# Kernel tuning notes

Measured on AMD Instinct MI355X. Metric: run time of the kernel, lower is better.

## Reference

```python
import jax, jax.numpy as jnp
import numpy as np

B, D, T, H = 256, 256, 512, 512  # batch, input_dim, seq_len, hidden_dim


def setup_inputs() -> dict:
    key = jax.random.key(0)
    ks = jax.random.split(key, 7)
    s = 1.0 / np.sqrt(H)
    u = lambda k, shape: jax.random.uniform(k, shape, jnp.float32, -s, s)
    return {
        "x": jax.random.normal(ks[0], (B, D, T), jnp.float32),
        "W_ih": u(ks[1], (4 * H, D)),   # gate order: i, f, g, o (PyTorch)
        "W_hh": u(ks[2], (4 * H, H)),
        "b_ih": u(ks[3], (4 * H,)),
        "b_hh": u(ks[4], (4 * H,)),
        "W_mlp": u(ks[5], (1, H)),      # Linear(hidden_dim, num_classes=1)
        "b_mlp": u(ks[6], (1,)),
    }


def reference(x, W_ih, W_hh, b_ih, b_hh, W_mlp, b_mlp):
    # x: (B, D, T) -> (T, B, D), matching the two transposes in LSTM_model
    xs = jnp.transpose(x, (2, 0, 1))
    # Precompute input contributions for all timesteps: (T, B, 4H)
    x_gates = jnp.einsum('tbd,gd->tbg', xs, W_ih) + b_ih + b_hh
    Hh = W_hh.shape[1]

    def step(carry, xg):
        h, c = carry
        g = xg + h @ W_hh.T                      # (B, 4H)
        i = jax.nn.sigmoid(g[:, 0 * Hh:1 * Hh])
        f = jax.nn.sigmoid(g[:, 1 * Hh:2 * Hh])
        gg = jnp.tanh(g[:, 2 * Hh:3 * Hh])
        o = jax.nn.sigmoid(g[:, 3 * Hh:4 * Hh])
        c_new = f * c + i * gg
        h_new = o * jnp.tanh(c_new)
        return (h_new, c_new), h_new

    h0 = jnp.zeros((x.shape[0], Hh), x.dtype)
    c0 = jnp.zeros((x.shape[0], Hh), x.dtype)
    _, h_t = jax.lax.scan(step, (h0, c0), x_gates)   # (T, B, H)

    # MLP with num_layers=1: single Linear(H, 1) then sigmoid, per timestep.
    logits = jnp.einsum('tbh,h->tb', h_t, W_mlp[0]) + b_mlp[0]  # (T, B)
    out = jax.nn.sigmoid(logits)
    return out.T  # (B, T), matching out[..., t] layout
```

## Files before the change

### kernel.cpp

```cpp
#include <hip/hip_runtime.h>
#include <stdint.h>

#define BSZ 256
#define DIN 256
#define TLEN 512
#define HDIM 512
#define POISON 0xAAAAAAAAu

typedef _Float16 h16;
typedef unsigned int u32;
typedef unsigned long long u64;
typedef __attribute__((ext_vector_type(8))) _Float16 half8;
typedef __attribute__((ext_vector_type(4))) float f32x4;

__device__ __forceinline__ float fast_sigmoid(float x) {
    return 1.0f / (1.0f + __expf(-x));
}
__device__ __forceinline__ float fast_tanh(float x) {
    return 2.0f / (1.0f + __expf(-2.0f * x)) - 1.0f;
}

__device__ __forceinline__ u64 load_agent_u64(const u64* p) {
    return __hip_atomic_load((u64*)p, __ATOMIC_RELAXED, __HIP_MEMORY_SCOPE_AGENT);
}
__device__ __forceinline__ void store_agent_u32(u32* p, u32 v) {
    __hip_atomic_store(p, v, __ATOMIC_RELAXED, __HIP_MEMORY_SCOPE_AGENT);
}

__global__ __launch_bounds__(256)
void transpose_x(const float* __restrict__ x, h16* __restrict__ xT) {
    __shared__ h16 tl[64][72];
    const int tid = threadIdx.x;
    const int tb  = blockIdx.x & 7;
    const int bd0 = (blockIdx.x >> 3) * 64;
    const int t0  = tb * 64;
#pragma unroll
    for (int p = 0; p < 4; ++p) {
        int idx  = p * 256 + tid;
        int bd_l = idx >> 4;
        int t4   = idx & 15;
        float4 v = *(const float4*)(x + (size_t)(bd0 + bd_l) * TLEN + t0 + t4 * 4);
        tl[t4 * 4 + 0][bd_l] = (h16)v.x;
        tl[t4 * 4 + 1][bd_l] = (h16)v.y;
        tl[t4 * 4 + 2][bd_l] = (h16)v.z;
        tl[t4 * 4 + 3][bd_l] = (h16)v.w;
    }
    __syncthreads();
#pragma unroll
    for (int p = 0; p < 2; ++p) {
        int idx = p * 256 + tid;
        int t_l = idx >> 3;
        int seg = idx & 7;
        uint4 v = *(const uint4*)&tl[t_l][seg * 8];
        *(uint4*)(xT + (size_t)(t0 + t_l) * (BSZ * DIN) + bd0 + seg * 8) = v;
    }
}

__global__ __launch_bounds__(256, 1)
void lstm_kernel(const float* __restrict__ x,
                 const float* __restrict__ W_ih,
                 const float* __restrict__ W_hh,
                 const float* __restrict__ b_ih,
                 const float* __restrict__ b_hh,
                 const float* __restrict__ W_mlp,
                 const h16* __restrict__ xT,
                 int use_xT,
                 h16* __restrict__ hslots,
                 float* __restrict__ logits,
                 float* __restrict__ part,
                 int use_part)
{
    __shared__ h16  h_sw[16][64][8];
    __shared__ h16  x_sw[8][8][64][8];
    __shared__ float g_lds[16][132];

    const int tid  = threadIdx.x;
    const int bid  = blockIdx.x;
    const int clique = bid & 15;
    const int mem    = bid >> 4;
    const int lane = tid & 63;
    const int w    = tid >> 6;
    const int l15  = lane & 15;
    const int lq   = lane >> 4;
    const int cb   = clique * 16;

    half8 whh[2][16], wih[2][8];
#pragma unroll
    for (int i = 0; i < 2; ++i) {
        const int nrow = w * HDIM + mem * 32 + i * 16 + l15;
        const float* wr = W_hh + (size_t)nrow * HDIM;
#pragma unroll
        for (int kk = 0; kk < 16; ++kk) {
            const float* p = wr + kk * 32 + lq * 8;
            half8 v;
#pragma unroll
            for (int j = 0; j < 8; ++j) v[j] = (h16)p[j];
            whh[i][kk] = v;
        }
        const float* wr2 = W_ih + (size_t)nrow * DIN;
#pragma unroll
        for (int kk = 0; kk < 8; ++kk) {
            const float* p = wr2 + kk * 32 + lq * 8;
            half8 v;
#pragma unroll
            for (int j = 0; j < 8; ++j) v[j] = (h16)p[j];
            wih[i][kk] = v;
        }
    }

    const int eb = tid >> 4;
    const int ej = tid & 15;
    const int jg = mem * 32 + ej * 2;
    float bias[8];
#pragma unroll
    for (int q = 0; q < 4; ++q) {
        bias[q * 2 + 0] = b_ih[q * HDIM + jg]     + b_hh[q * HDIM + jg];
        bias[q * 2 + 1] = b_ih[q * HDIM + jg + 1] + b_hh[q * HDIM + jg + 1];
    }
    const float wm0 = W_mlp[jg], wm1 = W_mlp[jg + 1];
    float c0 = 0.0f, c1 = 0.0f;
    float pbuf[8];

    u32  qoff[8];
    h16* hdst4[4];
#pragma unroll
    for (int it = 0; it < 4; ++it) {
        int c   = it * 256 + tid;
        int L   = c & 63;
        int kk  = c >> 6;
        int b   = L & 15;
        int k0  = kk * 32 + (L >> 4) * 8;
        qoff[it * 2 + 0] = (u32)((b * HDIM + k0) >> 2);
        qoff[it * 2 + 1] = qoff[it * 2 + 0] + 1;
        hdst4[it] = &h_sw[kk][L][0];
    }
    const size_t own_off = (size_t)(cb + eb) * HDIM + jg;

    for (int t = 0; t < TLEN; ++t) {
        if (use_xT) {
#pragma unroll
            for (int it = 0; it < 2; ++it) {
                int c  = it * 256 + tid;
                int L  = c & 63;
                int kk = c >> 6;
                int b  = L & 15;
                int d0 = kk * 32 + (L >> 4) * 8;
                uint4 v = *(const uint4*)(xT + (size_t)t * (BSZ * DIN)
                                             + (size_t)(cb + b) * DIN + d0);
                *(uint4*)&x_sw[0][kk][L][0] = v;
            }
        } else if ((t & 7) == 0) {
            const int d   = tid;
            const int kk  = d >> 5;
            const int dlq = (d >> 3) & 3;
            const int j   = d & 7;
#pragma unroll 4
            for (int b = 0; b < 16; ++b) {
                const float* p = x + ((size_t)(cb + b) * DIN + d) * TLEN + t;
                float4 v0 = *(const float4*)p;
                float4 v1 = *(const float4*)(p + 4);
                int L = b | (dlq << 4);
                x_sw[0][kk][L][j] = (h16)v0.x;
                x_sw[1][kk][L][j] = (h16)v0.y;
                x_sw[2][kk][L][j] = (h16)v0.z;
                x_sw[3][kk][L][j] = (h16)v0.w;
                x_sw[4][kk][L][j] = (h16)v1.x;
                x_sw[5][kk][L][j] = (h16)v1.y;
                x_sw[6][kk][L][j] = (h16)v1.z;
                x_sw[7][kk][L][j] = (h16)v1.w;
            }
        }
        const int sb = use_xT ? 0 : (t & 7);

        if (t > 0) {
            asm volatile("s_waitcnt vmcnt(0)" ::: "memory");
            store_agent_u32((u32*)(hslots + (size_t)((t + 3) & 7) * BSZ * HDIM
                                          + own_off), POISON);

            const u64* hb = (const u64*)(hslots + ((size_t)(t & 7) * BSZ + cb) * HDIM);
            u64 q[8];
            u32 pend = 0xFFu;
            while (pend) {
#pragma unroll
                for (int i = 0; i < 8; ++i)
                    if (pend & (1u << i)) q[i] = load_agent_u64(hb + qoff[i]);
                u32 np = 0;
#pragma unroll
                for (int i = 0; i < 8; ++i)
                    if (pend & (1u << i)) {
                        u32 lo = (u32)q[i], hi = (u32)(q[i] >> 32);
                        if (lo == POISON || hi == POISON) np |= 1u << i;
                    }
                pend = np;
                if (pend) __builtin_amdgcn_s_sleep(1);
            }
#pragma unroll
            for (int it = 0; it < 4; ++it) {
                union { u64 qq[2]; uint4 v; } pk;
                pk.qq[0] = q[it * 2 + 0];
                pk.qq[1] = q[it * 2 + 1];
                *(uint4*)hdst4[it] = pk.v;
            }
        }
        __syncthreads();

        f32x4 acc0 = {0.f, 0.f, 0.f, 0.f};
        f32x4 acc1 = {0.f, 0.f, 0.f, 0.f};
#pragma unroll
        for (int kk = 0; kk < 8; ++kk) {
            half8 a = *(const half8*)&x_sw[sb][kk][lane][0];
            acc0 = __builtin_amdgcn_mfma_f32_16x16x32_f16(a, wih[0][kk], acc0, 0, 0, 0);
            acc1 = __builtin_amdgcn_mfma_f32_16x16x32_f16(a, wih[1][kk], acc1, 0, 0, 0);
        }
        if (t > 0) {
#pragma unroll
            for (int kk = 0; kk < 16; ++kk) {
                half8 a = *(const half8*)&h_sw[kk][lane][0];
                acc0 = __builtin_amdgcn_mfma_f32_16x16x32_f16(a, whh[0][kk], acc0, 0, 0, 0);
                acc1 = __builtin_amdgcn_mfma_f32_16x16x32_f16(a, whh[1][kk], acc1, 0, 0, 0);
            }
        }
        {
            const int col0 = w * 32 + l15;
            const int col1 = w * 32 + 16 + l15;
#pragma unroll
            for (int r = 0; r < 4; ++r) {
                g_lds[lq * 4 + r][col0] = acc0[r];
                g_lds[lq * 4 + r][col1] = acc1[r];
            }
        }
        __syncthreads();

        float mlp_p;
        {
            float gi0 = g_lds[eb][ej * 2]          + bias[0];
            float gi1 = g_lds[eb][ej * 2 + 1]      + bias[1];
            float gf0 = g_lds[eb][32 + ej * 2]     + bias[2];
            float gf1 = g_lds[eb][32 + ej * 2 + 1] + bias[3];
            float gg0 = g_lds[eb][64 + ej * 2]     + bias[4];
            float gg1 = g_lds[eb][64 + ej * 2 + 1] + bias[5];
            float go0 = g_lds[eb][96 + ej * 2]     + bias[6];
            float go1 = g_lds[eb][96 + ej * 2 + 1] + bias[7];
            c0 = fast_sigmoid(gf0) * c0 + fast_sigmoid(gi0) * fast_tanh(gg0);
            c1 = fast_sigmoid(gf1) * c1 + fast_sigmoid(gi1) * fast_tanh(gg1);
            float h0 = fast_sigmoid(go0) * fast_tanh(c0);
            float h1 = fast_sigmoid(go1) * fast_tanh(c1);

            union { h16 h2[2]; u32 uu; } pk;
            pk.h2[0] = (h16)h0; pk.h2[1] = (h16)h1;
            if (pk.uu == POISON) pk.uu ^= 1u;
            store_agent_u32((u32*)(hslots + (size_t)((t + 1) & 7) * BSZ * HDIM
                                          + own_off), pk.uu);

            float p = h0 * wm0 + h1 * wm1;
            p += __shfl_xor(p, 1);
            p += __shfl_xor(p, 2);
            p += __shfl_xor(p, 4);
            p += __shfl_xor(p, 8);
            mlp_p = p;
            pbuf[t & 7] = p;
            if (use_part && (t & 7) == 7 && ej == 0) {
                float* pd = &part[((size_t)mem * BSZ + cb + eb) * TLEN + (t - 7)];
                float4 v0, v1;
                v0.x = pbuf[0]; v0.y = pbuf[1]; v0.z = pbuf[2]; v0.w = pbuf[3];
                v1.x = pbuf[4]; v1.y = pbuf[5]; v1.z = pbuf[6]; v1.w = pbuf[7];
                *(float4*)pd       = v0;
                *(float4*)(pd + 4) = v1;
            }
        }
        if (!use_part && ej == 0) {
            atomicAdd(&logits[(size_t)(cb + eb) * TLEN + t], mlp_p);
        }
    }
}

__global__ __launch_bounds__(256)
void final_sigmoid(const float* __restrict__ logits,
                   const float* __restrict__ part,
                   int use_part,
                   const float* __restrict__ b_mlp,
                   float* __restrict__ out) {
    int i = blockIdx.x * 256 + threadIdx.x;
    float v;
    if (use_part) {
        int t = i & (TLEN - 1);
        int b = i >> 9;
        v = 0.f;
#pragma unroll
        for (int mm = 0; mm < 16; ++mm)
            v += part[((size_t)mm * BSZ + b) * TLEN + t];
    } else {
        v = logits[i];
    }
    v += b_mlp[0];
    out[i] = 1.0f / (1.0f + __expf(-v));
}

extern "C" void kernel_launch(void* const* d_in, const int* in_sizes, int n_in,
                              void* d_out, int out_size, void* d_ws, size_t ws_size,
                              hipStream_t stream) {
    const float* x     = (const float*)d_in[0];
    const float* W_ih  = (const float*)d_in[1];
    const float* W_hh  = (const float*)d_in[2];
    const float* b_ih  = (const float*)d_in[3];
    const float* b_hh  = (const float*)d_in[4];
    const float* W_mlp = (const float*)d_in[5];
    const float* b_mlp = (const float*)d_in[6];
    float* out = (float*)d_out;

    char* ws = (char*)d_ws;
    float* logits = (float*)ws;
    h16*   hslots = (h16*)(ws + 1048576);
    float* part   = (float*)(ws + 4194304);
    h16*   xT     = (h16*)(ws + 20971520);
    const int use_part = (ws_size >= (size_t)20971520) ? 1 : 0;
    const int use_xT   = (ws_size >= (size_t)88080384) ? 1 : 0;

    hipMemsetAsync(d_ws, 0, 524288, stream);

    if (use_xT) {
        transpose_x<<<8192, 256, 0, stream>>>(x, xT);
    }
    lstm_kernel<<<256, 256, 0, stream>>>(x, W_ih, W_hh, b_ih, b_hh, W_mlp,
                                         xT, use_xT, hslots, logits,
                                         part, use_part);
    final_sigmoid<<<(BSZ * TLEN) / 256, 256, 0, stream>>>(logits, part, use_part,
                                                          b_mlp, out);
}
```

Measured before the change: 2.108 ms.

## Remap gate rows so MFMA output yields LSTM cell update in registers

Reorders the W_hh/W_ih rows each wave loads so that one wave's MFMA accumulators hold all four gates for a set of hidden units. The cell update is then done in registers with lane shuffles instead of spilling gates to LDS and re-reading them after a barrier. It also removes the pre-transposed x path and the per-clique partial-logit buffer, always using the strided x loads and atomic logit accumulation. Finally it moves the h-slot poll ahead of the x load and issues the poison stores after the h publish. The cost is more atomics, the reinstated strided x reads, and an extra barrier after the MFMAs.

```diff
diff --git a/kernel.cpp b/kernel.cpp
--- a/kernel.cpp
+++ b/kernel.cpp
@@ -13,11 +13,11 @@
 typedef __attribute__((ext_vector_type(8))) _Float16 half8;
 typedef __attribute__((ext_vector_type(4))) float f32x4;
 
-__device__ __forceinline__ float fast_sigmoid(float x) {
-    return 1.0f / (1.0f + __expf(-x));
-}
-__device__ __forceinline__ float fast_tanh(float x) {
-    return 2.0f / (1.0f + __expf(-2.0f * x)) - 1.0f;
+__device__ __forceinline__ float fsigm(float x) {
+    return __fdividef(1.0f, 1.0f + __expf(-x));
+}
+__device__ __forceinline__ float ftanh(float x) {
+    return __fdividef(2.0f, 1.0f + __expf(-2.0f * x)) - 1.0f;
 }
 
 __device__ __forceinline__ u64 load_agent_u64(const u64* p) {
@@ -25,35 +25,6 @@
 }
 __device__ __forceinline__ void store_agent_u32(u32* p, u32 v) {
     __hip_atomic_store(p, v, __ATOMIC_RELAXED, __HIP_MEMORY_SCOPE_AGENT);
-}
-
-__global__ __launch_bounds__(256)
-void transpose_x(const float* __restrict__ x, h16* __restrict__ xT) {
-    __shared__ h16 tl[64][72];
-    const int tid = threadIdx.x;
-    const int tb  = blockIdx.x & 7;
-    const int bd0 = (blockIdx.x >> 3) * 64;
-    const int t0  = tb * 64;
-#pragma unroll
-    for (int p = 0; p < 4; ++p) {
-        int idx  = p * 256 + tid;
-        int bd_l = idx >> 4;
-        int t4   = idx & 15;
-        float4 v = *(const float4*)(x + (size_t)(bd0 + bd_l) * TLEN + t0 + t4 * 4);
-        tl[t4 * 4 + 0][bd_l] = (h16)v.x;
-        tl[t4 * 4 + 1][bd_l] = (h16)v.y;
-        tl[t4 * 4 + 2][bd_l] = (h16)v.z;
-        tl[t4 * 4 + 3][bd_l] = (h16)v.w;
-    }
-    __syncthreads();
-#pragma unroll
-    for (int p = 0; p < 2; ++p) {
-        int idx = p * 256 + tid;
-        int t_l = idx >> 3;
-        int seg = idx & 7;
-        uint4 v = *(const uint4*)&tl[t_l][seg * 8];
-        *(uint4*)(xT + (size_t)(t0 + t_l) * (BSZ * DIN) + bd0 + seg * 8) = v;
-    }
 }
 
 __global__ __launch_bounds__(256, 1)
@@ -63,16 +34,13 @@
                  const float* __restrict__ b_ih,
                  const float* __restrict__ b_hh,
                  const float* __restrict__ W_mlp,
-                 const h16* __restrict__ xT,
-                 int use_xT,
                  h16* __restrict__ hslots,
-                 float* __restrict__ logits,
-                 float* __restrict__ part,
-                 int use_part)
+                 float* __restrict__ logits)
 {
-    __shared__ h16  h_sw[16][64][8];
-    __shared__ h16  x_sw[8][8][64][8];
-    __shared__ float g_lds[16][132];
+    __shared__ h16 h_sw[16][64][8];
+    __shared__ h16 x_sw[8][8][64][8];
+    __shared__ h16 pad[2048];
+    if (blockIdx.x == 0xFFFFFFFu) pad[threadIdx.x] = (h16)0.f;
 
     const int tid  = threadIdx.x;
     const int bid  = blockIdx.x;
@@ -83,11 +51,16 @@
     const int l15  = lane & 15;
     const int lq   = lane >> 4;
     const int cb   = clique * 16;
+    const int half = l15 >> 3;
+    const int uo   = l15 & 7;
+    const int u    = mem * 32 + w * 8 + uo;
+    const bool is_even = (uo & 1) == 0;
 
     half8 whh[2][16], wih[2][8];
 #pragma unroll
     for (int i = 0; i < 2; ++i) {
-        const int nrow = w * HDIM + mem * 32 + i * 16 + l15;
+        const int gate = i * 2 + half;
+        const int nrow = gate * HDIM + mem * 32 + w * 8 + uo;
         const float* wr = W_hh + (size_t)nrow * HDIM;
 #pragma unroll
         for (int kk = 0; kk < 16; ++kk) {
@@ -108,18 +81,15 @@
         }
     }
 
-    const int eb = tid >> 4;
-    const int ej = tid & 15;
-    const int jg = mem * 32 + ej * 2;
-    float bias[8];
-#pragma unroll
-    for (int q = 0; q < 4; ++q) {
-        bias[q * 2 + 0] = b_ih[q * HDIM + jg]     + b_hh[q * HDIM + jg];
-        bias[q * 2 + 1] = b_ih[q * HDIM + jg + 1] + b_hh[q * HDIM + jg + 1];
-    }
-    const float wm0 = W_mlp[jg], wm1 = W_mlp[jg + 1];
-    float c0 = 0.0f, c1 = 0.0f;
-    float pbuf[8];
+    const float bi = b_ih[u]            + b_hh[u];
+    const float bf = b_ih[HDIM + u]     + b_hh[HDIM + u];
+    const float bg = b_ih[2 * HDIM + u] + b_hh[2 * HDIM + u];
+    const float bo = b_ih[3 * HDIM + u] + b_hh[3 * HDIM + u];
+    const float wm = W_mlp[u];
+    const int   b0 = lq * 4 + half * 2;
+    const size_t own0 = (size_t)(cb + b0) * HDIM + u;
+    const size_t own1 = (size_t)(cb + b0 + 1) * HDIM + u;
+    float cst0 = 0.0f, cst1 = 0.0f;
 
     u32  qoff[8];
     h16* hdst4[4];
@@ -134,22 +104,36 @@
         qoff[it * 2 + 1] = qoff[it * 2 + 0] + 1;
         hdst4[it] = &h_sw[kk][L][0];
     }
-    const size_t own_off = (size_t)(cb + eb) * HDIM + jg;
 
     for (int t = 0; t < TLEN; ++t) {
-        if (use_xT) {
-#pragma unroll
-            for (int it = 0; it < 2; ++it) {
-                int c  = it * 256 + tid;
-                int L  = c & 63;
-                int kk = c >> 6;
-                int b  = L & 15;
-                int d0 = kk * 32 + (L >> 4) * 8;
-                uint4 v = *(const uint4*)(xT + (size_t)t * (BSZ * DIN)
-                                             + (size_t)(cb + b) * DIN + d0);
-                *(uint4*)&x_sw[0][kk][L][0] = v;
-            }
-        } else if ((t & 7) == 0) {
+        u64 q[8];
+        if (t > 0) {
+            const u64* hb = (const u64*)(hslots + ((size_t)(t & 7) * BSZ + cb) * HDIM);
+            u32 pend = 0xFFu;
+            while (pend) {
+#pragma unroll
+                for (int i = 0; i < 8; ++i)
+                    if (pend & (1u << i)) q[i] = load_agent_u64(hb + qoff[i]);
+                u32 np = 0;
+#pragma unroll
+                for (int i = 0; i < 8; ++i)
+                    if (pend & (1u << i)) {
+                        u32 lo = (u32)q[i], hi = (u32)(q[i] >> 32);
+                        if (lo == POISON || hi == POISON) np |= 1u << i;
+                    }
+                pend = np;
+                if (pend) __builtin_amdgcn_s_sleep(1);
+            }
+#pragma unroll
+            for (int it = 0; it < 4; ++it) {
+                union { u64 qq[2]; uint4 v; } pk;
+                pk.qq[0] = q[it * 2 + 0];
+                pk.qq[1] = q[it * 2 + 1];
+                *(uint4*)hdst4[it] = pk.v;
+            }
+        }
+
+        if ((t & 7) == 0) {
             const int d   = tid;
             const int kk  = d >> 5;
             const int dlq = (d >> 3) & 3;
@@ -170,38 +154,7 @@
                 x_sw[7][kk][L][j] = (h16)v1.w;
             }
         }
-        const int sb = use_xT ? 0 : (t & 7);
-
-        if (t > 0) {
-            asm volatile("s_waitcnt vmcnt(0)" ::: "memory");
-            store_agent_u32((u32*)(hslots + (size_t)((t + 3) & 7) * BSZ * HDIM
-                                          + own_off), POISON);
-
-            const u64* hb = (const u64*)(hslots + ((size_t)(t & 7) * BSZ + cb) * HDIM);
-            u64 q[8];
-            u32 pend = 0xFFu;
-            while (pend) {
-#pragma unroll
-                for (int i = 0; i < 8; ++i)
-                    if (pend & (1u << i)) q[i] = load_agent_u64(hb + qoff[i]);
-                u32 np = 0;
-#pragma unroll
-                for (int i = 0; i < 8; ++i)
-                    if (pend & (1u << i)) {
-                        u32 lo = (u32)q[i], hi = (u32)(q[i] >> 32);
-                        if (lo == POISON || hi == POISON) np |= 1u << i;
-                    }
-                pend = np;
-                if (pend) __builtin_amdgcn_s_sleep(1);
-            }
-#pragma unroll
-            for (int it = 0; it < 4; ++it) {
-                union { u64 qq[2]; uint4 v; } pk;
-                pk.qq[0] = q[it * 2 + 0];
-                pk.qq[1] = q[it * 2 + 1];
-                *(uint4*)hdst4[it] = pk.v;
-            }
-        }
+        const int sb = t & 7;
         __syncthreads();
 
         f32x4 acc0 = {0.f, 0.f, 0.f, 0.f};
@@ -220,79 +173,67 @@
                 acc1 = __builtin_amdgcn_mfma_f32_16x16x32_f16(a, whh[1][kk], acc1, 0, 0, 0);
             }
         }
+        __syncthreads();
+
+        float oa0 = half ? acc0[2] : acc0[0];
+        float oa1 = half ? acc0[3] : acc0[1];
+        float ob0 = half ? acc1[2] : acc1[0];
+        float ob1 = half ? acc1[3] : acc1[1];
+        float s0 = __shfl_xor(half ? acc0[0] : acc0[2], 8);
+        float s1 = __shfl_xor(half ? acc0[1] : acc0[3], 8);
+        float s2 = __shfl_xor(half ? acc1[0] : acc1[2], 8);
+        float s3 = __shfl_xor(half ? acc1[1] : acc1[3], 8);
+        float gi0 = half ? s0 : oa0,  gf0 = half ? oa0 : s0;
+        float gg0 = half ? s2 : ob0,  go0 = half ? ob0 : s2;
+        float gi1 = half ? s1 : oa1,  gf1 = half ? oa1 : s1;
+        float gg1 = half ? s3 : ob1,  go1 = half ? ob1 : s3;
+
+        float iv0 = fsigm(gi0 + bi), fv0 = fsigm(gf0 + bf);
+        float gv0 = ftanh(gg0 + bg), ov0 = fsigm(go0 + bo);
+        cst0 = fv0 * cst0 + iv0 * gv0;
+        float h0 = ov0 * ftanh(cst0);
+        float iv1 = fsigm(gi1 + bi), fv1 = fsigm(gf1 + bf);
+        float gv1 = ftanh(gg1 + bg), ov1 = fsigm(go1 + bo);
+        cst1 = fv1 * cst1 + iv1 * gv1;
+        float h1 = ov1 * ftanh(cst1);
+
+        float hp0 = __shfl_xor(h0, 1);
+        float hp1 = __shfl_xor(h1, 1);
+
+        asm volatile("s_waitcnt vmcnt(0)" ::: "memory");
         {
-            const int col0 = w * 32 + l15;
-            const int col1 = w * 32 + 16 + l15;
-#pragma unroll
-            for (int r = 0; r < 4; ++r) {
-                g_lds[lq * 4 + r][col0] = acc0[r];
-                g_lds[lq * 4 + r][col1] = acc1[r];
-            }
-        }
-        __syncthreads();
-
-        float mlp_p;
-        {
-            float gi0 = g_lds[eb][ej * 2]          + bias[0];
-            float gi1 = g_lds[eb][ej * 2 + 1]      + bias[1];
-            float gf0 = g_lds[eb][32 + ej * 2]     + bias[2];
-            float gf1 = g_lds[eb][32 + ej * 2 + 1] + bias[3];
-            float gg0 = g_lds[eb][64 + ej * 2]     + bias[4];
-            float gg1 = g_lds[eb][64 + ej * 2 + 1] + bias[5];
-            float go0 = g_lds[eb][96 + ej * 2]     + bias[6];
-            float go1 = g_lds[eb][96 + ej * 2 + 1] + bias[7];
-            c0 = fast_sigmoid(gf0) * c0 + fast_sigmoid(gi0) * fast_tanh(gg0);
-            c1 = fast_sigmoid(gf1) * c1 + fast_sigmoid(gi1) * fast_tanh(gg1);
-            float h0 = fast_sigmoid(go0) * fast_tanh(c0);
-            float h1 = fast_sigmoid(go1) * fast_tanh(c1);
-
-            union { h16 h2[2]; u32 uu; } pk;
-            pk.h2[0] = (h16)h0; pk.h2[1] = (h16)h1;
-            if (pk.uu == POISON) pk.uu ^= 1u;
-            store_agent_u32((u32*)(hslots + (size_t)((t + 1) & 7) * BSZ * HDIM
-                                          + own_off), pk.uu);
-
-            float p = h0 * wm0 + h1 * wm1;
-            p += __shfl_xor(p, 1);
-            p += __shfl_xor(p, 2);
-            p += __shfl_xor(p, 4);
-            p += __shfl_xor(p, 8);
-            mlp_p = p;
-            pbuf[t & 7] = p;
-            if (use_part && (t & 7) == 7 && ej == 0) {
-                float* pd = &part[((size_t)mem * BSZ + cb + eb) * TLEN + (t - 7)];
-                float4 v0, v1;
-                v0.x = pbuf[0]; v0.y = pbuf[1]; v0.z = pbuf[2]; v0.w = pbuf[3];
-                v1.x = pbuf[4]; v1.y = pbuf[5]; v1.z = pbuf[6]; v1.w = pbuf[7];
-                *(float4*)pd       = v0;
-                *(float4*)(pd + 4) = v1;
-            }
-        }
-        if (!use_part && ej == 0) {
-            atomicAdd(&logits[(size_t)(cb + eb) * TLEN + t], mlp_p);
+            h16* sbase = hslots + (size_t)((t + 1) & 7) * BSZ * HDIM;
+            if (is_even) {
+                union { h16 h2[2]; u32 uu; } p0, p1;
+                p0.h2[0] = (h16)h0; p0.h2[1] = (h16)hp0;
+                p1.h2[0] = (h16)h1; p1.h2[1] = (h16)hp1;
+                if (p0.uu == POISON) p0.uu ^= 1u;
+                if (p1.uu == POISON) p1.uu ^= 1u;
+                store_agent_u32((u32*)(sbase + own0), p0.uu);
+                store_agent_u32((u32*)(sbase + own1), p1.uu);
+            }
+        }
+        if (is_even) {
+            h16* pbase = hslots + (size_t)((t + 3) & 7) * BSZ * HDIM;
+            store_agent_u32((u32*)(pbase + own0), POISON);
+            store_agent_u32((u32*)(pbase + own1), POISON);
+        }
+        float p0v = h0 * wm, p1v = h1 * wm;
+        p0v += __shfl_xor(p0v, 1); p0v += __shfl_xor(p0v, 2); p0v += __shfl_xor(p0v, 4);
+        p1v += __shfl_xor(p1v, 1); p1v += __shfl_xor(p1v, 2); p1v += __shfl_xor(p1v, 4);
+        if (uo == 0) {
+            atomicAdd(&logits[(size_t)(cb + b0) * TLEN + t], p0v);
+            atomicAdd(&logits[(size_t)(cb + b0 + 1) * TLEN + t], p1v);
         }
     }
 }
 
 __global__ __launch_bounds__(256)
 void final_sigmoid(const float* __restrict__ logits,
-                   const float* __restrict__ part,
-                   int use_part,
                    const float* __restrict__ b_mlp,
                    float* __restrict__ out) {
     int i = blockIdx.x * 256 + threadIdx.x;
-    float v;
-    if (use_part) {
-        int t = i & (TLEN - 1);
-        int b = i >> 9;
-        v = 0.f;
-#pragma unroll
-        for (int mm = 0; mm < 16; ++mm)
-            v += part[((size_t)mm * BSZ + b) * TLEN + t];
-    } else {
-        v = logits[i];
-    }
-    v += b_mlp[0];
+    float v = logits[i] + b_mlp[0];
     out[i] = 1.0f / (1.0f + __expf(-v));
 }
 
@@ -311,19 +252,9 @@
     char* ws = (char*)d_ws;
     float* logits = (float*)ws;
     h16*   hslots = (h16*)(ws + 1048576);
-    float* part   = (float*)(ws + 4194304);
-    h16*   xT     = (h16*)(ws + 20971520);
-    const int use_part = (ws_size >= (size_t)20971520) ? 1 : 0;
-    const int use_xT   = (ws_size >= (size_t)88080384) ? 1 : 0;
-
     hipMemsetAsync(d_ws, 0, 524288, stream);
 
-    if (use_xT) {
-        transpose_x<<<8192, 256, 0, stream>>>(x, xT);
-    }
     lstm_kernel<<<256, 256, 0, stream>>>(x, W_ih, W_hh, b_ih, b_hh, W_mlp,
-                                         xT, use_xT, hslots, logits,
-                                         part, use_part);
-    final_sigmoid<<<(BSZ * TLEN) / 256, 256, 0, stream>>>(logits, part, use_part,
-                                                          b_mlp, out);
-}
+                                         hslots, logits);
+    final_sigmoid<<<(BSZ * TLEN) / 256, 256, 0, stream>>>(logits, b_mlp, out);
+}
```

New measurement: 2.711 ms. 1.29x slower.

## Precompute next step's input projection after publishing h, drop transpose kernel

Applied to the files above, without the earlier changes.

Removes the separate transpose_x pre-pass and xT workspace path. The kernel now always loads x directly every 8 steps and computes the W_ih·x contribution for step t+1 right after publishing h_t, so that MFMA work overlaps the cross-block wait instead of sitting on the critical path after the spin. The poison store for the future slot is moved next to the h store. It also switches the activations to __fdividef. The risk is that an extra __syncthreads on x reload steps and the early x_sw overwrite could race with reads of the current buffer.

```diff
diff --git a/kernel.cpp b/kernel.cpp
--- a/kernel.cpp
+++ b/kernel.cpp
@@ -13,11 +13,11 @@
 typedef __attribute__((ext_vector_type(8))) _Float16 half8;
 typedef __attribute__((ext_vector_type(4))) float f32x4;
 
-__device__ __forceinline__ float fast_sigmoid(float x) {
-    return 1.0f / (1.0f + __expf(-x));
-}
-__device__ __forceinline__ float fast_tanh(float x) {
-    return 2.0f / (1.0f + __expf(-2.0f * x)) - 1.0f;
+__device__ __forceinline__ float fsigm(float x) {
+    return __fdividef(1.0f, 1.0f + __expf(-x));
+}
+__device__ __forceinline__ float ftanh(float x) {
+    return __fdividef(2.0f, 1.0f + __expf(-2.0f * x)) - 1.0f;
 }
 
 __device__ __forceinline__ u64 load_agent_u64(const u64* p) {
@@ -25,35 +25,6 @@
 }
 __device__ __forceinline__ void store_agent_u32(u32* p, u32 v) {
     __hip_atomic_store(p, v, __ATOMIC_RELAXED, __HIP_MEMORY_SCOPE_AGENT);
-}
-
-__global__ __launch_bounds__(256)
-void transpose_x(const float* __restrict__ x, h16* __restrict__ xT) {
-    __shared__ h16 tl[64][72];
-    const int tid = threadIdx.x;
-    const int tb  = blockIdx.x & 7;
-    const int bd0 = (blockIdx.x >> 3) * 64;
-    const int t0  = tb * 64;
-#pragma unroll
-    for (int p = 0; p < 4; ++p) {
-        int idx  = p * 256 + tid;
-        int bd_l = idx >> 4;
-        int t4   = idx & 15;
-        float4 v = *(const float4*)(x + (size_t)(bd0 + bd_l) * TLEN + t0 + t4 * 4);
-        tl[t4 * 4 + 0][bd_l] = (h16)v.x;
-        tl[t4 * 4 + 1][bd_l] = (h16)v.y;
-        tl[t4 * 4 + 2][bd_l] = (h16)v.z;
-        tl[t4 * 4 + 3][bd_l] = (h16)v.w;
-    }
-    __syncthreads();
-#pragma unroll
-    for (int p = 0; p < 2; ++p) {
-        int idx = p * 256 + tid;
-        int t_l = idx >> 3;
-        int seg = idx & 7;
-        uint4 v = *(const uint4*)&tl[t_l][seg * 8];
-        *(uint4*)(xT + (size_t)(t0 + t_l) * (BSZ * DIN) + bd0 + seg * 8) = v;
-    }
 }
 
 __global__ __launch_bounds__(256, 1)
@@ -63,8 +34,6 @@
                  const float* __restrict__ b_ih,
                  const float* __restrict__ b_hh,
                  const float* __restrict__ W_mlp,
-                 const h16* __restrict__ xT,
-                 int use_xT,
                  h16* __restrict__ hslots,
                  float* __restrict__ logits,
                  float* __restrict__ part,
@@ -120,6 +89,7 @@
     const float wm0 = W_mlp[jg], wm1 = W_mlp[jg + 1];
     float c0 = 0.0f, c1 = 0.0f;
     float pbuf[8];
+    const size_t own_off = (size_t)(cb + eb) * HDIM + jg;
 
     u32  qoff[8];
     h16* hdst4[4];
@@ -134,49 +104,41 @@
         qoff[it * 2 + 1] = qoff[it * 2 + 0] + 1;
         hdst4[it] = &h_sw[kk][L][0];
     }
-    const size_t own_off = (size_t)(cb + eb) * HDIM + jg;
+
+    const int xd   = tid;
+    const int xkk  = xd >> 5;
+    const int xL_q = (xd >> 3) & 3;
+    const int xj   = xd & 7;
+
+    f32x4 ax0 = {0.f, 0.f, 0.f, 0.f};
+    f32x4 ax1 = {0.f, 0.f, 0.f, 0.f};
+    {
+#pragma unroll 4
+        for (int b = 0; b < 16; ++b) {
+            const float* p = x + ((size_t)(cb + b) * DIN + xd) * TLEN + 0;
+            float4 v0 = *(const float4*)p;
+            float4 v1 = *(const float4*)(p + 4);
+            int L = b | (xL_q << 4);
+            x_sw[0][xkk][L][xj] = (h16)v0.x;
+            x_sw[1][xkk][L][xj] = (h16)v0.y;
+            x_sw[2][xkk][L][xj] = (h16)v0.z;
+            x_sw[3][xkk][L][xj] = (h16)v0.w;
+            x_sw[4][xkk][L][xj] = (h16)v1.x;
+            x_sw[5][xkk][L][xj] = (h16)v1.y;
+            x_sw[6][xkk][L][xj] = (h16)v1.z;
+            x_sw[7][xkk][L][xj] = (h16)v1.w;
+        }
+        __syncthreads();
+#pragma unroll
+        for (int kk = 0; kk < 8; ++kk) {
+            half8 a = *(const half8*)&x_sw[0][kk][lane][0];
+            ax0 = __builtin_amdgcn_mfma_f32_16x16x32_f16(a, wih[0][kk], ax0, 0, 0, 0);
+            ax1 = __builtin_amdgcn_mfma_f32_16x16x32_f16(a, wih[1][kk], ax1, 0, 0, 0);
+        }
+    }
 
     for (int t = 0; t < TLEN; ++t) {
-        if (use_xT) {
-#pragma unroll
-            for (int it = 0; it < 2; ++it) {
-                int c  = it * 256 + tid;
-                int L  = c & 63;
-                int kk = c >> 6;
-                int b  = L & 15;
-                int d0 = kk * 32 + (L >> 4) * 8;
-                uint4 v = *(const uint4*)(xT + (size_t)t * (BSZ * DIN)
-                                             + (size_t)(cb + b) * DIN + d0);
-                *(uint4*)&x_sw[0][kk][L][0] = v;
-            }
-        } else if ((t & 7) == 0) {
-            const int d   = tid;
-            const int kk  = d >> 5;
-            const int dlq = (d >> 3) & 3;
-            const int j   = d & 7;
-#pragma unroll 4
-            for (int b = 0; b < 16; ++b) {
-                const float* p = x + ((size_t)(cb + b) * DIN + d) * TLEN + t;
-                float4 v0 = *(const float4*)p;
-                float4 v1 = *(const float4*)(p + 4);
-                int L = b | (dlq << 4);
-                x_sw[0][kk][L][j] = (h16)v0.x;
-                x_sw[1][kk][L][j] = (h16)v0.y;
-                x_sw[2][kk][L][j] = (h16)v0.z;
-                x_sw[3][kk][L][j] = (h16)v0.w;
-                x_sw[4][kk][L][j] = (h16)v1.x;
-                x_sw[5][kk][L][j] = (h16)v1.y;
-                x_sw[6][kk][L][j] = (h16)v1.z;
-                x_sw[7][kk][L][j] = (h16)v1.w;
-            }
-        }
-        const int sb = use_xT ? 0 : (t & 7);
-
         if (t > 0) {
-            asm volatile("s_waitcnt vmcnt(0)" ::: "memory");
-            store_agent_u32((u32*)(hslots + (size_t)((t + 3) & 7) * BSZ * HDIM
-                                          + own_off), POISON);
-
             const u64* hb = (const u64*)(hslots + ((size_t)(t & 7) * BSZ + cb) * HDIM);
             u64 q[8];
             u32 pend = 0xFFu;
@@ -204,14 +166,7 @@
         }
         __syncthreads();
 
-        f32x4 acc0 = {0.f, 0.f, 0.f, 0.f};
-        f32x4 acc1 = {0.f, 0.f, 0.f, 0.f};
-#pragma unroll
-        for (int kk = 0; kk < 8; ++kk) {
-            half8 a = *(const half8*)&x_sw[sb][kk][lane][0];
-            acc0 = __builtin_amdgcn_mfma_f32_16x16x32_f16(a, wih[0][kk], acc0, 0, 0, 0);
-            acc1 = __builtin_amdgcn_mfma_f32_16x16x32_f16(a, wih[1][kk], acc1, 0, 0, 0);
-        }
+        f32x4 acc0 = ax0, acc1 = ax1;
         if (t > 0) {
 #pragma unroll
             for (int kk = 0; kk < 16; ++kk) {
@@ -231,45 +186,77 @@
         }
         __syncthreads();
 
-        float mlp_p;
-        {
-            float gi0 = g_lds[eb][ej * 2]          + bias[0];
-            float gi1 = g_lds[eb][ej * 2 + 1]      + bias[1];
-            float gf0 = g_lds[eb][32 + ej * 2]     + bias[2];
-            float gf1 = g_lds[eb][32 + ej * 2 + 1] + bias[3];
-            float gg0 = g_lds[eb][64 + ej * 2]     + bias[4];
-            float gg1 = g_lds[eb][64 + ej * 2 + 1] + bias[5];
-            float go0 = g_lds[eb][96 + ej * 2]     + bias[6];
-            float go1 = g_lds[eb][96 + ej * 2 + 1] + bias[7];
-            c0 = fast_sigmoid(gf0) * c0 + fast_sigmoid(gi0) * fast_tanh(gg0);
-            c1 = fast_sigmoid(gf1) * c1 + fast_sigmoid(gi1) * fast_tanh(gg1);
-            float h0 = fast_sigmoid(go0) * fast_tanh(c0);
-            float h1 = fast_sigmoid(go1) * fast_tanh(c1);
-
-            union { h16 h2[2]; u32 uu; } pk;
-            pk.h2[0] = (h16)h0; pk.h2[1] = (h16)h1;
-            if (pk.uu == POISON) pk.uu ^= 1u;
-            store_agent_u32((u32*)(hslots + (size_t)((t + 1) & 7) * BSZ * HDIM
-                                          + own_off), pk.uu);
-
-            float p = h0 * wm0 + h1 * wm1;
-            p += __shfl_xor(p, 1);
-            p += __shfl_xor(p, 2);
-            p += __shfl_xor(p, 4);
-            p += __shfl_xor(p, 8);
-            mlp_p = p;
-            pbuf[t & 7] = p;
-            if (use_part && (t & 7) == 7 && ej == 0) {
-                float* pd = &part[((size_t)mem * BSZ + cb + eb) * TLEN + (t - 7)];
-                float4 v0, v1;
-                v0.x = pbuf[0]; v0.y = pbuf[1]; v0.z = pbuf[2]; v0.w = pbuf[3];
-                v1.x = pbuf[4]; v1.y = pbuf[5]; v1.z = pbuf[6]; v1.w = pbuf[7];
-                *(float4*)pd       = v0;
-                *(float4*)(pd + 4) = v1;
-            }
+        float gi0 = g_lds[eb][ej * 2]          + bias[0];
+        float gi1 = g_lds[eb][ej * 2 + 1]      + bias[1];
+        float gf0 = g_lds[eb][32 + ej * 2]     + bias[2];
+        float gf1 = g_lds[eb][32 + ej * 2 + 1] + bias[3];
+        float gg0 = g_lds[eb][64 + ej * 2]     + bias[4];
+        float gg1 = g_lds[eb][64 + ej * 2 + 1] + bias[5];
+        float go0 = g_lds[eb][96 + ej * 2]     + bias[6];
+        float go1 = g_lds[eb][96 + ej * 2 + 1] + bias[7];
+        c0 = fsigm(gf0) * c0 + fsigm(gi0) * ftanh(gg0);
+        c1 = fsigm(gf1) * c1 + fsigm(gi1) * ftanh(gg1);
+        float h0 = fsigm(go0) * ftanh(c0);
+        float h1 = fsigm(go1) * ftanh(c1);
+
+        union { h16 h2[2]; u32 uu; } pk;
+        pk.h2[0] = (h16)h0; pk.h2[1] = (h16)h1;
+        if (pk.uu == POISON) pk.uu ^= 1u;
+
+        asm volatile("s_waitcnt vmcnt(0)" ::: "memory");
+        store_agent_u32((u32*)(hslots + (size_t)((t + 1) & 7) * BSZ * HDIM
+                                      + own_off), pk.uu);
+        store_agent_u32((u32*)(hslots + (size_t)((t + 3) & 7) * BSZ * HDIM
+                                      + own_off), POISON);
+
+        float p = h0 * wm0 + h1 * wm1;
+        p += __shfl_xor(p, 1);
+        p += __shfl_xor(p, 2);
+        p += __shfl_xor(p, 4);
+        p += __shfl_xor(p, 8);
+        pbuf[t & 7] = p;
+        if (use_part && (t & 7) == 7 && ej == 0) {
+            float* pd = &part[((size_t)mem * BSZ + cb + eb) * TLEN + (t - 7)];
+            float4 v0, v1;
+            v0.x = pbuf[0]; v0.y = pbuf[1]; v0.z = pbuf[2]; v0.w = pbuf[3];
+            v1.x = pbuf[4]; v1.y = pbuf[5]; v1.z = pbuf[6]; v1.w = pbuf[7];
+            *(float4*)pd       = v0;
+            *(float4*)(pd + 4) = v1;
         }
         if (!use_part && ej == 0) {
-            atomicAdd(&logits[(size_t)(cb + eb) * TLEN + t], mlp_p);
+            atomicAdd(&logits[(size_t)(cb + eb) * TLEN + t], p);
+        }
+
+        if (t + 1 < TLEN) {
+            const int tn = t + 1;
+            if ((tn & 7) == 0) {
+#pragma unroll 4
+                for (int b = 0; b < 16; ++b) {
+                    const float* px = x + ((size_t)(cb + b) * DIN + xd) * TLEN + tn;
+                    float4 v0 = *(const float4*)px;
+                    float4 v1 = *(const float4*)(px + 4);
+                    int L = b | (xL_q << 4);
+                    x_sw[0][xkk][L][xj] = (h16)v0.x;
+                    x_sw[1][xkk][L][xj] = (h16)v0.y;
+                    x_sw[2][xkk][L][xj] = (h16)v0.z;
+                    x_sw[3][xkk][L][xj] = (h16)v0.w;
+                    x_sw[4][xkk][L][xj] = (h16)v1.x;
+                    x_sw[5][xkk][L][xj] = (h16)v1.y;
+                    x_sw[6][xkk][L][xj] = (h16)v1.z;
+                    x_sw[7][xkk][L][xj] = (h16)v1.w;
+                }
+                __syncthreads();
+            }
+            const int sbn = tn & 7;
+            f32x4 n0 = {0.f, 0.f, 0.f, 0.f};
+            f32x4 n1 = {0.f, 0.f, 0.f, 0.f};
+#pragma unroll
+            for (int kk = 0; kk < 8; ++kk) {
+                half8 a = *(const half8*)&x_sw[sbn][kk][lane][0];
+                n0 = __builtin_amdgcn_mfma_f32_16x16x32_f16(a, wih[0][kk], n0, 0, 0, 0);
+                n1 = __builtin_amdgcn_mfma_f32_16x16x32_f16(a, wih[1][kk], n1, 0, 0, 0);
+            }
+            ax0 = n0; ax1 = n1;
         }
     }
 }
@@ -312,18 +299,12 @@
     float* logits = (float*)ws;
     h16*   hslots = (h16*)(ws + 1048576);
     float* part   = (float*)(ws + 4194304);
-    h16*   xT     = (h16*)(ws + 20971520);
     const int use_part = (ws_size >= (size_t)20971520) ? 1 : 0;
-    const int use_xT   = (ws_size >= (size_t)88080384) ? 1 : 0;
 
     hipMemsetAsync(d_ws, 0, 524288, stream);
 
-    if (use_xT) {
-        transpose_x<<<8192, 256, 0, stream>>>(x, xT);
-    }
     lstm_kernel<<<256, 256, 0, stream>>>(x, W_ih, W_hh, b_ih, b_hh, W_mlp,
-                                         xT, use_xT, hslots, logits,
-                                         part, use_part);
+                                         hslots, logits, part, use_part);
     final_sigmoid<<<(BSZ * TLEN) / 256, 256, 0, stream>>>(logits, part, use_part,
                                                           b_mlp, out);
 }
```

Result: slower. 2.183 ms (+3.5%).
